# Kernel tuning notes

Measured on AMD Instinct MI355X. Metric: run time of the kernel, lower is better.

## Reference

```python
import jax, jax.numpy as jnp
import numpy as np

ALPHA = 3.0      # tanhalpha
K = 10           # subgraph_size (overridden to 10 in __init__)
PROP_ALPHA = 0.05
DEPTH = 2        # gcn_depth
NUM_FEAT = 2


def _build_graph(emb1, emb2, w1, b1, w2, b2):
    # MTGNN graph_constructor: directed adjacency + row-wise top-k sparsification
    n1 = jnp.tanh(ALPHA * (emb1 @ w1 + b1))
    n2 = jnp.tanh(ALPHA * (emb2 @ w2 + b2))
    a = n1 @ n2.T - n2 @ n1.T
    adj = jax.nn.relu(jnp.tanh(ALPHA * a))          # [N, N]
    _, idx = jax.lax.top_k(adj, K)                  # keep top-K per row
    N = adj.shape[0]
    mask = jnp.zeros_like(adj).at[jnp.arange(N)[:, None], idx].set(1.0)
    return adj * mask


def _norm_adj(adj):
    a = adj + jnp.eye(adj.shape[0], dtype=adj.dtype)
    return a / a.sum(axis=1, keepdims=True)


def _mixprop(x, a_norm, w, b):
    # x: [B, C, N, L]; multi-hop diffusion then 1x1 conv over stacked hops
    h = x
    outs = [x]
    for _ in range(DEPTH):
        h = PROP_ALPHA * x + (1.0 - PROP_ALPHA) * jnp.einsum('bcwl,vw->bcvl', h, a_norm)
        outs.append(h)
    ho = jnp.concatenate(outs, axis=1)              # [B, (D+1)C, N, L]
    return jnp.einsum('bcnl,oc->bonl', ho, w) + b[None, :, None, None]


def _conv1x1(x, w, b):
    # 1x1 Conv2d over channel dim of [B, C, N, L]
    return jnp.einsum('bcnl,oc->bonl', x, w) + b[None, :, None, None]


def _forward(history_data, node_emb_u, T_i_D_emb, D_i_W_emb,
             gc_emb1, gc_emb2, gc_w1, gc_b1, gc_w2, gc_b2,
             W_emb, b_emb, Wg1, bg1, Wg2, bg2, Wsc, bsc,
             mix1_w, mix1_b, mix2_w, mix2_b,
             Wtf1, btf1, Wtf2, btf2, Wec1, bec1, Wec2, bec2,
             Wfc1, bfc1, Wfc2, bfc2, Wec3, bec3):
    # --- prepare inputs ---
    tid_idx = (history_data[..., NUM_FEAT] * 288.0).astype(jnp.int32)   # [B,T,N]
    diw_idx = history_data[..., NUM_FEAT + 1].astype(jnp.int32)
    tid = T_i_D_emb[tid_idx]                                            # [B,T,N,TE]
    diw = D_i_W_emb[diw_idx]                                            # [B,T,N,TE]
    hd = history_data[..., :NUM_FEAT]                                   # [B,T,N,F]

    adj = _build_graph(gc_emb1, gc_emb2, gc_w1, gc_b1, gc_w2, gc_b2)    # [N,N]

    hd = hd @ W_emb + b_emb                                             # [B,T,N,H]
    B, T, N, H = hd.shape

    # --- decouple gate 1 ---
    nu = jnp.broadcast_to(node_emb_u[None, None], (B, T, N, node_emb_u.shape[-1]))
    g_in = jnp.concatenate([nu, tid, diw], axis=-1)                     # [B,T,N,64]
    gate = jax.nn.sigmoid(jax.nn.relu(g_in @ Wg1 + bg1) @ Wg2 + bg2)    # [B,T,N,H]
    x1 = gate * hd
    x2 = hd - x1
    gated = jnp.concatenate([x1, x2], axis=-1)                          # [B,T,N,2H]

    # start conv acts on the T(=12) dim as channels
    x1 = jax.nn.relu(jnp.einsum('btnh,ot->bonh', x1, Wsc) + bsc[None, :, None, None])
    x2 = jax.nn.relu(jnp.einsum('btnh,ot->bonh', x2, Wsc) + bsc[None, :, None, None])

    aN = _norm_adj(adj)
    aTN = _norm_adj(adj.T)
    outs = []
    for i in range(2):
        H1 = _mixprop(x1, aN, mix1_w[i], mix1_b[i]) + _mixprop(x1, aTN, mix2_w[i], mix2_b[i])
        H2 = _mixprop(x2, aN, mix1_w[i], mix1_b[i]) + _mixprop(x2, aTN, mix2_w[i], mix2_b[i])
        outs.append(H1)
        outs.append(H2)
    out = jnp.concatenate(outs, axis=-1)                                # [B,32,N,4H]

    # TFModule: 2-layer MLP on last dim (dropout = identity in eval)
    x = jax.nn.relu(out @ Wtf1 + btf1) @ Wtf2 + btf2                    # [B,32,N,4H]

    x = jax.nn.relu(_conv1x1(x, Wec1, bec1))                            # [B,128,N,4H]
    x = _conv1x1(x, Wec2, bec2)                                         # [B,12,N,4H]

    fh = jnp.concatenate([gated, x, tid, diw, hd], axis=-1)             # [B,12,N,472]
    f = jax.nn.relu(jax.nn.relu(fh) @ Wfc1 + bfc1) @ Wfc2 + bfc2        # [B,12,N,gap]
    f = _conv1x1(f, Wec3, bec3)                                         # [B,4,N,gap]
    f = jnp.transpose(f, (0, 2, 1, 3)).reshape(B, N, -1)                # [B,N,12]
    return f


def setup_inputs() -> dict:
    key = jax.random.key(0)
    ks = iter(jax.random.split(key, 48))
    def p(*shape, s=0.1):
        return (jax.random.normal(next(ks), shape, jnp.float32) * s)
    B, T, N, F_, H, ND, TE = 8, 12, 1024, 2, 64, 40, 12
    feat = jax.random.normal(next(ks), (B, T, N, F_), jnp.float32)
    tid = jax.random.uniform(next(ks), (B, T, N, 1), jnp.float32)
    diw = jax.random.randint(next(ks), (B, T, N, 1), 0, 7).astype(jnp.float32)
    history_data = jnp.concatenate([feat, tid, diw], axis=-1)
    return {
        'history_data': history_data,
        'node_emb_u': p(N, ND), 'T_i_D_emb': p(288, TE), 'D_i_W_emb': p(7, TE),
        'gc_emb1': p(N, ND), 'gc_emb2': p(N, ND),
        'gc_w1': p(ND, ND), 'gc_b1': jnp.zeros((ND,), jnp.float32),
        'gc_w2': p(ND, ND), 'gc_b2': jnp.zeros((ND,), jnp.float32),
        'W_emb': p(F_, H), 'b_emb': jnp.zeros((H,), jnp.float32),
        'Wg1': p(ND + 2 * TE, 64), 'bg1': jnp.zeros((64,), jnp.float32),
        'Wg2': p(64, H), 'bg2': jnp.zeros((H,), jnp.float32),
        'Wsc': p(32, T), 'bsc': jnp.zeros((32,), jnp.float32),
        'mix1_w': p(2, 32, 96), 'mix1_b': jnp.zeros((2, 32), jnp.float32),
        'mix2_w': p(2, 32, 96), 'mix2_b': jnp.zeros((2, 32), jnp.float32),
        'Wtf1': p(4 * H, 256, s=0.05), 'btf1': jnp.zeros((256,), jnp.float32),
        'Wtf2': p(256, 4 * H, s=0.05), 'btf2': jnp.zeros((4 * H,), jnp.float32),
        'Wec1': p(128, 32), 'bec1': jnp.zeros((128,), jnp.float32),
        'Wec2': p(12, 128), 'bec2': jnp.zeros((12,), jnp.float32),
        'Wfc1': p(472, 512, s=0.05), 'bfc1': jnp.zeros((512,), jnp.float32),
        'Wfc2': p(512, 3, s=0.05), 'bfc2': jnp.zeros((3,), jnp.float32),
        'Wec3': p(4, 12), 'bec3': jnp.zeros((4,), jnp.float32),
    }


def reference(history_data, node_emb_u, T_i_D_emb, D_i_W_emb,
              gc_emb1, gc_emb2, gc_w1, gc_b1, gc_w2, gc_b2,
              W_emb, b_emb, Wg1, bg1, Wg2, bg2, Wsc, bsc,
              mix1_w, mix1_b, mix2_w, mix2_b,
              Wtf1, btf1, Wtf2, btf2, Wec1, bec1, Wec2, bec2,
              Wfc1, bfc1, Wfc2, bfc2, Wec3, bec3):
    return _forward(history_data, node_emb_u, T_i_D_emb, D_i_W_emb,
                    gc_emb1, gc_emb2, gc_w1, gc_b1, gc_w2, gc_b2,
                    W_emb, b_emb, Wg1, bg1, Wg2, bg2, Wsc, bsc,
                    mix1_w, mix1_b, mix2_w, mix2_b,
                    Wtf1, btf1, Wtf2, btf2, Wec1, bec1, Wec2, bec2,
                    Wfc1, bfc1, Wfc2, bfc2, Wec3, bec3)
```

## Files before the change

kernel.cpp:

```cpp
#include <hip/hip_runtime.h>
#include <math.h>

constexpr int ROWS_PER_B = 12 * 1024;

constexpr size_t F_N1 = 0;
constexpr size_t F_N2 = 40960;
constexpr size_t F_ANVAL = 81920;
constexpr size_t F_ROWVAL = 93184;
constexpr size_t F_COLSUM = 103424;
constexpr size_t F_INVCS = 104448;
constexpr size_t F_ATVAL = 105472;
constexpr size_t I_ANIDX = 115712;
constexpr size_t I_ROWIDX = 126976;
constexpr size_t I_COLCNT = 137216;
constexpr size_t I_COLOFF = 138240;
constexpr size_t I_COLFILL = 139265;
constexpr size_t I_ATIDX = 140289;
constexpr size_t F_W1P = 151552;
constexpr size_t F_W2P = 184320;
constexpr size_t F_WFCP = 217088;
constexpr size_t F_WEC1P = 339968;
constexpr size_t F_WEC2P = 342016;
constexpr size_t F_WMWP = 343040;
constexpr size_t GRAPH_FLOATS = 524288;

constexpr size_t PB_GATED = (size_t)ROWS_PER_B * 128 / 2;
constexpr size_t PB_HD = (size_t)ROWS_PER_B * 64 / 2;
constexpr size_t PB_X = (size_t)32 * 1024 * 64 / 2;
constexpr size_t PB_MIX = (size_t)32 * 1024 * 256 / 2;
constexpr size_t PB_APK = (size_t)768 * 15 * 64 * 8 / 2;
constexpr size_t PB_TOTAL = PB_GATED + PB_HD + 5 * PB_X + PB_MIX + PB_APK;

typedef __attribute__((ext_vector_type(8))) short bf16x8;
typedef __attribute__((ext_vector_type(4))) float f32x4;

__device__ __forceinline__ unsigned short f2bf(float f) {
    unsigned u = __float_as_uint(f);
    unsigned r = (u + 0x7fffu + ((u >> 16) & 1u)) >> 16;
    return (unsigned short)r;
}
__device__ __forceinline__ float bf2f(unsigned short h) {
    return __uint_as_float((unsigned)h << 16);
}
__device__ __forceinline__ void unpack8(uint4 raw, float* f) {
    f[0] = bf2f((unsigned short)(raw.x & 0xffff)); f[1] = bf2f((unsigned short)(raw.x >> 16));
    f[2] = bf2f((unsigned short)(raw.y & 0xffff)); f[3] = bf2f((unsigned short)(raw.y >> 16));
    f[4] = bf2f((unsigned short)(raw.z & 0xffff)); f[5] = bf2f((unsigned short)(raw.z >> 16));
    f[6] = bf2f((unsigned short)(raw.w & 0xffff)); f[7] = bf2f((unsigned short)(raw.w >> 16));
}
__device__ __forceinline__ uint4 pack8(const float* f) {
    uint4 r;
    r.x = f2bf(f[0]) | ((unsigned)f2bf(f[1]) << 16);
    r.y = f2bf(f[2]) | ((unsigned)f2bf(f[3]) << 16);
    r.z = f2bf(f[4]) | ((unsigned)f2bf(f[5]) << 16);
    r.w = f2bf(f[6]) | ((unsigned)f2bf(f[7]) << 16);
    return r;
}
__device__ __forceinline__ bf16x8 relu8(bf16x8 v) {
#pragma unroll
    for (int j = 0; j < 8; j++) {
        unsigned short u = (unsigned short)v[j];
        v[j] = (short)((u >> 15) ? 0 : u);
    }
    return v;
}


__global__ void k_init(int* cnt, int* fill, float* csum) {
    int t = blockIdx.x * 256 + threadIdx.x;
    if (t < 1024) { cnt[t] = 0; fill[t] = 0; csum[t] = 0.f; }
}

__global__ void k_embed(const float* e1, const float* e2, const float* w1, const float* b1,
                        const float* w2, const float* b2, float* n1, float* n2) {
    int idx = blockIdx.x * 256 + threadIdx.x;
    if (idx >= 81920) return;
    int m = idx / 40960, rem = idx - m * 40960;
    int i = rem / 40, j = rem - i * 40;
    const float* e = m ? e2 : e1;
    const float* w = m ? w2 : w1;
    const float* bv = m ? b2 : b1;
    float a = bv[j];
    for (int k = 0; k < 40; k++) a += e[i * 40 + k] * w[k * 40 + j];
    (m ? n2 : n1)[i * 40 + j] = tanhf(3.0f * a);
}

__global__ __launch_bounds__(256) void k_adj(const float* n1, const float* n2,
        float* aN_val, int* aN_idx, float* row_val, int* row_idx,
        int* col_cnt, float* col_sum) {
    __shared__ float arow[1024];
    __shared__ float n1v[40], n2v[40];
    __shared__ float rv[256];
    __shared__ int ri[256];
    __shared__ float topv[10];
    __shared__ int topi[10];
    int v = blockIdx.x, t = threadIdx.x;
    if (t < 40) { n1v[t] = n1[v * 40 + t]; n2v[t] = n2[v * 40 + t]; }
    __syncthreads();
    for (int j = t; j < 1024; j += 256) {
        float d1 = 0.f, d2 = 0.f;
        for (int k = 0; k < 40; k++) {
            d1 += n1v[k] * n2[j * 40 + k];
            d2 += n2v[k] * n1[j * 40 + k];
        }
        float a = tanhf(3.0f * (d1 - d2));
        arow[j] = a > 0.f ? a : 0.f;
    }
    __syncthreads();
    for (int r = 0; r < 10; r++) {
        float bv = -1.f; int bi = 1 << 30;
        for (int j = t; j < 1024; j += 256) {
            float x = arow[j];
            if (x > bv || (x == bv && j < bi)) { bv = x; bi = j; }
        }
        rv[t] = bv; ri[t] = bi;
        __syncthreads();
        for (int s = 128; s > 0; s >>= 1) {
            if (t < s) {
                float ov = rv[t + s]; int oi = ri[t + s];
                if (ov > rv[t] || (ov == rv[t] && oi < ri[t])) { rv[t] = ov; ri[t] = oi; }
            }
            __syncthreads();
        }
        if (t == 0) { topv[r] = rv[0]; topi[r] = ri[0]; arow[ri[0]] = -1.f; }
        __syncthreads();
    }
    if (t == 0) {
        float s = 1.f;
        for (int r = 0; r < 10; r++) s += topv[r];
        float inv = 1.f / s;
        for (int r = 0; r < 10; r++) {
            aN_idx[v * 11 + r] = topi[r];
            aN_val[v * 11 + r] = topv[r] * inv;
            row_idx[v * 10 + r] = topi[r];
            row_val[v * 10 + r] = topv[r];
            atomicAdd(&col_cnt[topi[r]], 1);
            atomicAdd(&col_sum[topi[r]], topv[r]);
        }
        aN_idx[v * 11 + 10] = v;
        aN_val[v * 11 + 10] = inv;
    }
}

__global__ __launch_bounds__(1024) void k_scan(const int* cnt, int* off,
                                               const float* csum, float* inv) {
    __shared__ int tmp[1024];
    int t = threadIdx.x;
    tmp[t] = cnt[t];
    __syncthreads();
    for (int s = 1; s < 1024; s <<= 1) {
        int v = 0;
        if (t >= s) v = tmp[t - s];
        __syncthreads();
        tmp[t] += v;
        __syncthreads();
    }
    off[t + 1] = tmp[t];
    if (t == 0) off[0] = 0;
    inv[t] = 1.0f / (csum[t] + 1.0f);
}

__global__ void k_scatter(const int* row_idx, const float* row_val, const int* off,
                          int* fill, int* aT_idx, float* aT_val) {
    int e = blockIdx.x * 256 + threadIdx.x;
    if (e >= 10240) return;
    int v = e / 10;
    int j = row_idx[e];
    int pos = off[j] + atomicAdd(&fill[j], 1);
    aT_idx[pos] = v;
    aT_val[pos] = row_val[e];
}

__global__ void k_packw(const float* W, unsigned short* out) {
    int id = blockIdx.x * 256 + threadIdx.x;
    if (id >= 8192) return;
    int lane = id & 63, rest = id >> 6;
    int nb = rest & 15, kb = rest >> 4;
    int krow = kb * 32 + (lane >> 4) * 8;
    int col = nb * 16 + (lane & 15);
    unsigned short v[8];
#pragma unroll
    for (int j = 0; j < 8; j++) v[j] = f2bf(W[(size_t)(krow + j) * 256 + col]);
#pragma unroll
    for (int j = 0; j < 8; j++) out[(size_t)id * 8 + j] = v[j];
}

__global__ void k_packfc(const float* W, unsigned short* out) {
    int id = blockIdx.x * 256 + threadIdx.x;
    if (id >= 30720) return;
    int lane = id & 63, rest = id >> 6;
    int nb = rest & 31, kb = rest >> 5;
    int k0 = kb * 32 + (lane >> 4) * 8;
    int col = nb * 16 + (lane & 15);
    unsigned short v[8];
#pragma unroll
    for (int j = 0; j < 8; j++) {
        int k = k0 + j;
        v[j] = (k < 472) ? f2bf(W[(size_t)k * 512 + col]) : (unsigned short)0;
    }
#pragma unroll
    for (int j = 0; j < 8; j++) out[(size_t)id * 8 + j] = v[j];
}

__global__ void k_packec(const float* W1, const float* W2,
                         unsigned short* o1, unsigned short* o2) {
    int id = blockIdx.x * 256 + threadIdx.x;
    if (id < 512) {
        int mt = id >> 6, lane = id & 63;
        int o = mt * 16 + (lane & 15);
        int c0 = (lane >> 4) * 8;
#pragma unroll
        for (int j = 0; j < 8; j++)
            o1[(size_t)id * 8 + j] = f2bf(W1[o * 32 + c0 + j]);
    } else if (id < 768) {
        int id2 = id - 512;
        int kb = id2 >> 6, lane = id2 & 63;
        int p = lane & 15;
        int k0 = kb * 32 + (lane >> 4) * 8;
#pragma unroll
        for (int j = 0; j < 8; j++)
            o2[(size_t)id2 * 8 + j] = (p < 12) ? f2bf(W2[p * 128 + k0 + j])
                                               : (unsigned short)0;
    }
}

__global__ void k_packmw(const float* mw1, const float* mw2, unsigned short* out) {
    int id = blockIdx.x * 256 + threadIdx.x;
    if (id >= 1536) return;
    int f = id >> 6, lane = id & 63;
    int kb = f >> 2, rt = f & 3;
    int row = rt * 16 + (lane & 15);
    int ph = (kb >= 3) ? 1 : 0;
    int kloc = (kb - ph * 3) * 32 + (lane >> 4) * 8;
    const float* mw = ph ? mw2 : mw1;
#pragma unroll
    for (int j = 0; j < 8; j++)
        out[(size_t)id * 8 + j] = f2bf(mw[row * 96 + kloc + j]);
}


__global__ __launch_bounds__(256) void k_gate(const float* hist, const float* nodeu,
        const float* tide, const float* diwe,
        const float* Wg1, const float* bg1, const float* Wg2, const float* bg2,
        const float* Wemb, const float* bemb, unsigned short* gated, unsigned short* hd_emb) {
    __shared__ float w1[4096], w2[4096];
    __shared__ float gin[4][64], hid[4][64];
    __shared__ float sb1[64], sb2[64], we[128], be[64];
    int t = threadIdx.x;
    for (int i = t; i < 4096; i += 256) { w1[i] = Wg1[i]; w2[i] = Wg2[i]; }
    if (t < 64) { sb1[t] = bg1[t]; sb2[t] = bg2[t]; be[t] = bemb[t]; }
    if (t < 128) we[t] = Wemb[t];
    int r = t >> 6, lane = t & 63;
    int row = blockIdx.x * 4 + r;
    int n = row & 1023;
    const float* hrow = hist + (size_t)row * 4;
    float f0 = hrow[0], f1 = hrow[1];
    int tid_i = (int)(hrow[2] * 288.0f);
    int diw_i = (int)hrow[3];
    float g;
    if (lane < 40) g = nodeu[n * 40 + lane];
    else if (lane < 52) g = tide[tid_i * 12 + lane - 40];
    else g = diwe[diw_i * 12 + lane - 52];
    gin[r][lane] = g;
    __syncthreads();
    float acc = sb1[lane];
    for (int k = 0; k < 64; k++) acc += gin[r][k] * w1[k * 64 + lane];
    hid[r][lane] = acc > 0.f ? acc : 0.f;
    __syncthreads();
    acc = sb2[lane];
    for (int k = 0; k < 64; k++) acc += hid[r][k] * w2[k * 64 + lane];
    float gate = 1.f / (1.f + expf(-acc));
    float hd = f0 * we[lane] + f1 * we[64 + lane] + be[lane];
    float x1 = gate * hd;
    gated[(size_t)row * 128 + lane] = f2bf(x1);
    gated[(size_t)row * 128 + 64 + lane] = f2bf(hd - x1);
    hd_emb[(size_t)row * 64 + lane] = f2bf(hd);
}

__global__ __launch_bounds__(256) void k_wsc(const unsigned short* gated, const float* Wsc,
                                             const float* bsc, unsigned short* xs, int xoff) {
    __shared__ float w[384];
    __shared__ float sb[32];
    int t = threadIdx.x;
    if (t < 384) w[t] = Wsc[t];
    if (t < 32) sb[t] = bsc[t];
    __syncthreads();
    int idx = blockIdx.x * 256 + t;
    int h = idx & 63, n = (idx >> 6) & 1023, b = idx >> 16;
    float xv[12];
#pragma unroll
    for (int tt = 0; tt < 12; tt++)
        xv[tt] = bf2f(gated[(size_t)((b * 12 + tt) * 1024 + n) * 128 + xoff + h]);
#pragma unroll
    for (int o = 0; o < 32; o++) {
        float a = sb[o];
#pragma unroll
        for (int tt = 0; tt < 12; tt++) a += xv[tt] * w[o * 12 + tt];
        xs[(size_t)((b * 32 + o) * 1024 + n) * 64 + h] = f2bf(a > 0.f ? a : 0.f);
    }
}

__global__ __launch_bounds__(256) void k_spmm2(unsigned short* out1, unsigned short* out2,
        const unsigned short* x, const unsigned short* hin1, const unsigned short* hin2,
        const int* aN_idx, const float* aN_val,
        const int* aT_idx, const float* aT_val,
        const int* off, const float* inv_cs) {
    int nper = gridDim.x >> 3;
    int bid = (blockIdx.x & 7) * nper + (blockIdx.x >> 3);
    int t = threadIdx.x;
    int l8 = t & 7, r = t >> 3;
    int g = bid * 32 + r;
    int v = g & 1023, bc = g >> 10;
    size_t rowoff = (size_t)bc * 65536;
    float hv[8];
    const unsigned short* base1 = hin1 + rowoff;
    float s1[8];
#pragma unroll
    for (int j = 0; j < 8; j++) s1[j] = 0.f;
#pragma unroll
    for (int e = 0; e < 11; e++) {
        int w = aN_idx[v * 11 + e];
        float a = aN_val[v * 11 + e];
        uint4 raw = *(const uint4*)(base1 + (size_t)w * 64 + l8 * 8);
        unpack8(raw, hv);
#pragma unroll
        for (int j = 0; j < 8; j++) s1[j] += a * hv[j];
    }
    const unsigned short* base2 = hin2 + rowoff;
    float s2[8];
    {
        uint4 raw = *(const uint4*)(base2 + (size_t)v * 64 + l8 * 8);
        unpack8(raw, s2);
        int e0 = off[v], e1 = off[v + 1];
        for (int e = e0; e < e1; e++) {
            int w = aT_idx[e];
            float a = aT_val[e];
            uint4 rw = *(const uint4*)(base2 + (size_t)w * 64 + l8 * 8);
            unpack8(rw, hv);
#pragma unroll
            for (int j = 0; j < 8; j++) s2[j] += a * hv[j];
        }
        float ic = inv_cs[v];
#pragma unroll
        for (int j = 0; j < 8; j++) s2[j] *= ic;
    }
    uint4 xr = *(const uint4*)(x + (size_t)g * 64 + l8 * 8);
    float xv[8];
    unpack8(xr, xv);
    float o1[8], o2[8];
#pragma unroll
    for (int j = 0; j < 8; j++) {
        float xb = 0.05f * xv[j];
        o1[j] = xb + 0.95f * s1[j];
        o2[j] = xb + 0.95f * s2[j];
    }
    *(uint4*)(out1 + (size_t)g * 64 + l8 * 8) = pack8(o1);
    *(uint4*)(out2 + (size_t)g * 64 + l8 * 8) = pack8(o2);
}

__global__ __launch_bounds__(256) void k_proj(const unsigned short* xs,
        const unsigned short* h1, const unsigned short* h2,
        const unsigned short* h1b, const unsigned short* h2b,
        const unsigned short* mwp, const float* m1b, const float* m2b,
        unsigned short* mix, int xp) {
    __shared__ unsigned short Bf[24 * 64 * 8];
    int t = threadIdx.x;
    int wave = t >> 6, l = t & 63;
    int lr = l & 15, lg = l >> 4;
    int b = blockIdx.x >> 10, n = blockIdx.x & 1023;
#pragma unroll
    for (int i = 0; i < 6; i++) {
        int f = wave * 6 + i;
        int kb = f >> 2, nt = f & 3;
        int ph = (kb >= 3) ? 1 : 0;
        int q = kb - ph * 3;
        const unsigned short* Hq = (q == 0) ? xs : (q == 1 ? (ph ? h1b : h1)
                                                           : (ph ? h2b : h2));
        const unsigned short* src = Hq + ((size_t)(b * 32 + lg * 8) * 1024 + n) * 64
                                       + nt * 16 + lr;
        bf16x8 v;
#pragma unroll
        for (int j = 0; j < 8; j++)
            v[j] = (short)src[(size_t)j * 65536];
        *(bf16x8*)(Bf + ((size_t)f * 64 + l) * 8) = v;
    }
    __syncthreads();
    f32x4 acc[4];
#pragma unroll
    for (int nt = 0; nt < 4; nt++) {
        f32x4 c;
#pragma unroll
        for (int r = 0; r < 4; r++) {
            int row = wave * 16 + lg * 4 + r;
            c[r] = m1b[row] + m2b[row];
        }
        acc[nt] = c;
    }
#pragma unroll
    for (int kb = 0; kb < 6; kb++) {
        bf16x8 af = *(const bf16x8*)(mwp + (size_t)((kb * 4 + wave) * 64 + l) * 8);
#pragma unroll
        for (int nt = 0; nt < 4; nt++) {
            bf16x8 bfv = *(const bf16x8*)(Bf + ((size_t)(kb * 4 + nt) * 64 + l) * 8);
            acc[nt] = __builtin_amdgcn_mfma_f32_16x16x32_bf16(af, bfv, acc[nt], 0, 0, 0);
        }
    }
#pragma unroll
    for (int nt = 0; nt < 4; nt++)
#pragma unroll
        for (int r = 0; r < 4; r++) {
            int row = wave * 16 + lg * 4 + r;
            int i2 = row >> 5, o = row & 31;
            mix[(size_t)((b * 32 + o) * 1024 + n) * 256 + (i2 * 2 + xp) * 64 + nt * 16 + lr]
                = f2bf(acc[nt][r]);
        }
}

__global__ __launch_bounds__(256) void k_tf(unsigned short* mix, const unsigned short* W1p,
                                            const float* B1, const unsigned short* W2p,
                                            const float* B2) {
    __shared__ unsigned short Abuf[32 * 256];
    __shared__ unsigned short Hbuf[32 * 256];
    int t = threadIdx.x;
    int wave = t >> 6, l = t & 63;
    size_t row0 = (size_t)blockIdx.x * 32;
    const uint4* src = (const uint4*)(mix + row0 * 256);
#pragma unroll
    for (int it = 0; it < 4; it++) {
        int f = t + it * 256;
        uint4 raw = src[f];
        int e = f * 8, row = e >> 8, col = e & 255;
        int byte = (row * 512 + col * 2) ^ ((row & 7) << 4);
        *(uint4*)((char*)Abuf + byte) = raw;
    }
    __syncthreads();
    int colg0 = wave * 64;
    int lr = l & 15, lg = l >> 4;
    f32x4 acc[2][4];
#pragma unroll
    for (int nb = 0; nb < 4; nb++) {
        float bv = B1[colg0 + nb * 16 + lr];
        f32x4 c; c[0] = bv; c[1] = bv; c[2] = bv; c[3] = bv;
        acc[0][nb] = c; acc[1][nb] = c;
    }
#pragma unroll
    for (int kb = 0; kb < 8; kb++) {
        int k2 = (kb * 32 + lg * 8) * 2;
        int by0 = (lr * 512 + k2) ^ ((lr & 7) << 4);
        int by1 = ((16 + lr) * 512 + k2) ^ ((lr & 7) << 4);
        bf16x8 a0 = *(const bf16x8*)((char*)Abuf + by0);
        bf16x8 a1 = *(const bf16x8*)((char*)Abuf + by1);
#pragma unroll
        for (int nb = 0; nb < 4; nb++) {
            int nbg = wave * 4 + nb;
            bf16x8 bw = *(const bf16x8*)(W1p + (size_t)((kb * 16 + nbg) * 64 + l) * 8);
            acc[0][nb] = __builtin_amdgcn_mfma_f32_16x16x32_bf16(a0, bw, acc[0][nb], 0, 0, 0);
            acc[1][nb] = __builtin_amdgcn_mfma_f32_16x16x32_bf16(a1, bw, acc[1][nb], 0, 0, 0);
        }
    }
#pragma unroll
    for (int rb = 0; rb < 2; rb++)
#pragma unroll
        for (int nb = 0; nb < 4; nb++)
#pragma unroll
            for (int r = 0; r < 4; r++) {
                int row = rb * 16 + lg * 4 + r;
                int col = colg0 + nb * 16 + lr;
                unsigned short h = f2bf(fmaxf(acc[rb][nb][r], 0.f));
                int byte = (row * 512 + col * 2) ^ ((row & 7) << 4);
                *(unsigned short*)((char*)Hbuf + byte) = h;
            }
    __syncthreads();
#pragma unroll
    for (int nb = 0; nb < 4; nb++) {
        float bv = B2[colg0 + nb * 16 + lr];
        f32x4 c; c[0] = bv; c[1] = bv; c[2] = bv; c[3] = bv;
        acc[0][nb] = c; acc[1][nb] = c;
    }
#pragma unroll
    for (int kb = 0; kb < 8; kb++) {
        int k2 = (kb * 32 + lg * 8) * 2;
        int by0 = (lr * 512 + k2) ^ ((lr & 7) << 4);
        int by1 = ((16 + lr) * 512 + k2) ^ ((lr & 7) << 4);
        bf16x8 a0 = *(const bf16x8*)((char*)Hbuf + by0);
        bf16x8 a1 = *(const bf16x8*)((char*)Hbuf + by1);
#pragma unroll
        for (int nb = 0; nb < 4; nb++) {
            int nbg = wave * 4 + nb;
            bf16x8 bw = *(const bf16x8*)(W2p + (size_t)((kb * 16 + nbg) * 64 + l) * 8);
            acc[0][nb] = __builtin_amdgcn_mfma_f32_16x16x32_bf16(a0, bw, acc[0][nb], 0, 0, 0);
            acc[1][nb] = __builtin_amdgcn_mfma_f32_16x16x32_bf16(a1, bw, acc[1][nb], 0, 0, 0);
        }
    }
#pragma unroll
    for (int rb = 0; rb < 2; rb++)
#pragma unroll
        for (int nb = 0; nb < 4; nb++)
#pragma unroll
            for (int r = 0; r < 4; r++) {
                int row = rb * 16 + lg * 4 + r;
                int col = colg0 + nb * 16 + lr;
                mix[(row0 + row) * 256 + col] = f2bf(acc[rb][nb][r]);
            }
}

__global__ __launch_bounds__(256) void k_ec(const unsigned short* tfo,
        const unsigned short* W1p, const float* B1,
        const unsigned short* W2p, const float* B2, unsigned short* eco) {
    __shared__ unsigned short Hl[4 * 64 * 48];
    int t = threadIdx.x;
    int wave = t >> 6, l = t & 63;
    int lr = l & 15, lg = l >> 4;
    int b = blockIdx.x >> 10, n = blockIdx.x & 1023;
    int lbase = wave * 64;
    unsigned short* myH = Hl + wave * 3072;
    const unsigned short* xb = tfo + ((size_t)(b * 32) * 1024 + n) * 256;
    bf16x8 xf[4];
#pragma unroll
    for (int nt = 0; nt < 4; nt++) {
        int ll = lbase + nt * 16 + lr;
        bf16x8 v;
#pragma unroll
        for (int j = 0; j < 8; j++)
            v[j] = (short)xb[(size_t)(lg * 8 + j) * 262144 + ll];
        xf[nt] = v;
    }
    f32x4 d2[4];
    {
        f32x4 c;
#pragma unroll
        for (int r = 0; r < 4; r++) {
            int p = lg * 4 + r;
            c[r] = (p < 12) ? B2[p] : 0.f;
        }
#pragma unroll
        for (int nt = 0; nt < 4; nt++) d2[nt] = c;
    }
#pragma unroll
    for (int ch = 0; ch < 4; ch++) {
        f32x4 h[2][4];
#pragma unroll
        for (int mt = 0; mt < 2; mt++) {
            f32x4 c;
#pragma unroll
            for (int r = 0; r < 4; r++) c[r] = B1[ch * 32 + mt * 16 + lg * 4 + r];
#pragma unroll
            for (int nt = 0; nt < 4; nt++) h[mt][nt] = c;
        }
#pragma unroll
        for (int mt = 0; mt < 2; mt++) {
            bf16x8 aw = *(const bf16x8*)(W1p + (size_t)((ch * 2 + mt) * 64 + l) * 8);
#pragma unroll
            for (int nt = 0; nt < 4; nt++)
                h[mt][nt] = __builtin_amdgcn_mfma_f32_16x16x32_bf16(aw, xf[nt], h[mt][nt], 0, 0, 0);
        }
#pragma unroll
        for (int mt = 0; mt < 2; mt++)
#pragma unroll
            for (int nt = 0; nt < 4; nt++) {
                unsigned lo = f2bf(fmaxf(h[mt][nt][0], 0.f)) |
                              ((unsigned)f2bf(fmaxf(h[mt][nt][1], 0.f)) << 16);
                unsigned hi = f2bf(fmaxf(h[mt][nt][2], 0.f)) |
                              ((unsigned)f2bf(fmaxf(h[mt][nt][3], 0.f)) << 16);
                uint2 pk; pk.x = lo; pk.y = hi;
                *(uint2*)(myH + (nt * 16 + lr) * 48 + mt * 16 + lg * 4) = pk;
            }
        bf16x8 aw2 = *(const bf16x8*)(W2p + (size_t)(ch * 64 + l) * 8);
#pragma unroll
        for (int nt = 0; nt < 4; nt++) {
            bf16x8 hf = *(const bf16x8*)(myH + (nt * 16 + lr) * 48 + lg * 8);
            d2[nt] = __builtin_amdgcn_mfma_f32_16x16x32_bf16(aw2, hf, d2[nt], 0, 0, 0);
        }
    }
#pragma unroll
    for (int nt = 0; nt < 4; nt++)
#pragma unroll
        for (int r = 0; r < 4; r++) {
            int p = lg * 4 + r;
            if (p < 12) {
                int ll = lbase + nt * 16 + lr;
                eco[((size_t)(b * 12 + p) * 1024 + n) * 256 + ll] = f2bf(d2[nt][r]);
            }
        }
}

__global__ __launch_bounds__(256) void k_stage(const unsigned short* gated,
        const unsigned short* eco, const unsigned short* hd_emb,
        const float* hist, const float* tide, const float* diwe,
        unsigned short* apk) {
    int id = blockIdx.x * 256 + threadIdx.x;
    int lane = id & 63, rest = id >> 6;
    int rg = rest / 15, kb = rest - rg * 15;
    int lr = lane & 15, lg = lane >> 4;
    int grow = rg * 16 + lr;
    int n = grow & 1023, bt = grow >> 10;
    int b = bt / 12, tt = bt - b * 12;
    int off = kb * 32 + lg * 8;
    bf16x8 v;
    if (kb <= 3) {
        v = relu8(*(const bf16x8*)(gated + (size_t)grow * 128 + off));
    } else if (kb <= 11) {
        v = relu8(*(const bf16x8*)(eco + (size_t)((b * 12 + tt) * 1024 + n) * 256 + off - 128));
    } else if (kb == 12) {
        int tid_i = (int)(hist[(size_t)grow * 4 + 2] * 288.0f);
        int diw_i = (int)hist[(size_t)grow * 4 + 3];
        const unsigned short* hptr = hd_emb + (size_t)grow * 64;
#pragma unroll
        for (int j = 0; j < 8; j++) {
            int k = off + j;
            float x;
            if (k < 396) x = tide[tid_i * 12 + k - 384];
            else if (k < 408) x = diwe[diw_i * 12 + k - 396];
            else x = bf2f(hptr[k - 408]);
            v[j] = (short)f2bf(fmaxf(x, 0.f));
        }
    } else if (kb == 13) {
        v = relu8(*(const bf16x8*)(hd_emb + (size_t)grow * 64 + off - 408));
    } else {
        if (lg < 3) v = relu8(*(const bf16x8*)(hd_emb + (size_t)grow * 64 + off - 408));
        else {
#pragma unroll
            for (int j = 0; j < 8; j++) v[j] = 0;
        }
    }
    *(bf16x8*)(apk + (size_t)id * 8) = v;
}

__global__ __launch_bounds__(256) void k_fc(const unsigned short* apk,
        const unsigned short* W1p, const float* B1, const float* W2,
        float* pbuf) {
    int t = threadIdx.x;
    int wave = t >> 6, l = t & 63;
    int lr = l & 15, lg = l >> 4;
    int rg = blockIdx.x;
    int row0 = rg * 16;
    int colg0 = wave * 128;
    f32x4 acc[8];
#pragma unroll
    for (int nb = 0; nb < 8; nb++) {
        float bv = B1[colg0 + nb * 16 + lr];
        f32x4 c; c[0] = bv; c[1] = bv; c[2] = bv; c[3] = bv;
        acc[nb] = c;
    }
#pragma unroll
    for (int kb = 0; kb < 15; kb++) {
        bf16x8 af = *(const bf16x8*)(apk + (size_t)((rg * 15 + kb) * 64 + l) * 8);
#pragma unroll
        for (int nb = 0; nb < 8; nb++) {
            bf16x8 bw = *(const bf16x8*)(W1p + (size_t)((kb * 32 + wave * 8 + nb) * 64 + l) * 8);
            acc[nb] = __builtin_amdgcn_mfma_f32_16x16x32_bf16(af, bw, acc[nb], 0, 0, 0);
        }
    }
    float p[4][3];
#pragma unroll
    for (int r = 0; r < 4; r++) { p[r][0] = 0.f; p[r][1] = 0.f; p[r][2] = 0.f; }
#pragma unroll
    for (int nb = 0; nb < 8; nb++) {
        int col = colg0 + nb * 16 + lr;
        float w0 = W2[col * 3], w1 = W2[col * 3 + 1], w2 = W2[col * 3 + 2];
#pragma unroll
        for (int r = 0; r < 4; r++) {
            float h = fmaxf(acc[nb][r], 0.f);
            p[r][0] += h * w0; p[r][1] += h * w1; p[r][2] += h * w2;
        }
    }
#pragma unroll
    for (int off = 8; off >= 1; off >>= 1)
#pragma unroll
        for (int r = 0; r < 4; r++) {
            p[r][0] += __shfl_xor(p[r][0], off);
            p[r][1] += __shfl_xor(p[r][1], off);
            p[r][2] += __shfl_xor(p[r][2], off);
        }
    if (lr == 0) {
#pragma unroll
        for (int r = 0; r < 4; r++) {
            size_t gr = (size_t)(row0 + lg * 4 + r);
#pragma unroll
            for (int pp = 0; pp < 3; pp++)
                pbuf[gr * 12 + wave * 3 + pp] = p[r][pp];
        }
    }
}

__global__ void k_ec3(const float* pbuf, const float* B2, const float* W, const float* bv,
                      float* out) {
    int idx = blockIdx.x * 256 + threadIdx.x;
    int l = idx % 3;
    int rest = idx / 3;
    int o = rest & 3;
    int n = (rest >> 2) & 1023;
    int b = rest >> 12;
    float s = bv[o];
#pragma unroll
    for (int c = 0; c < 12; c++) {
        const float* pb = pbuf + ((size_t)(b * 12 + c) * 1024 + n) * 12;
        float fv = B2[l] + pb[l] + pb[3 + l] + pb[6 + l] + pb[9 + l];
        s += fv * W[o * 12 + c];
    }
    out[idx] = s;
}

extern "C" void kernel_launch(void* const* d_in, const int* in_sizes, int n_in,
                              void* d_out, int out_size, void* d_ws, size_t ws_size,
                              hipStream_t stream) {
    const float* hist = (const float*)d_in[0];
    const float* node_emb_u = (const float*)d_in[1];
    const float* T_i_D_emb = (const float*)d_in[2];
    const float* D_i_W_emb = (const float*)d_in[3];
    const float* gc_emb1 = (const float*)d_in[4];
    const float* gc_emb2 = (const float*)d_in[5];
    const float* gc_w1 = (const float*)d_in[6];
    const float* gc_b1 = (const float*)d_in[7];
    const float* gc_w2 = (const float*)d_in[8];
    const float* gc_b2 = (const float*)d_in[9];
    const float* W_emb = (const float*)d_in[10];
    const float* b_emb = (const float*)d_in[11];
    const float* Wg1 = (const float*)d_in[12];
    const float* bg1 = (const float*)d_in[13];
    const float* Wg2 = (const float*)d_in[14];
    const float* bg2 = (const float*)d_in[15];
    const float* Wsc = (const float*)d_in[16];
    const float* bsc = (const float*)d_in[17];
    const float* mix1_w = (const float*)d_in[18];
    const float* mix1_b = (const float*)d_in[19];
    const float* mix2_w = (const float*)d_in[20];
    const float* mix2_b = (const float*)d_in[21];
    const float* Wtf1 = (const float*)d_in[22];
    const float* btf1 = (const float*)d_in[23];
    const float* Wtf2 = (const float*)d_in[24];
    const float* btf2 = (const float*)d_in[25];
    const float* Wec1 = (const float*)d_in[26];
    const float* bec1 = (const float*)d_in[27];
    const float* Wec2 = (const float*)d_in[28];
    const float* bec2 = (const float*)d_in[29];
    const float* Wfc1 = (const float*)d_in[30];
    const float* bfc1 = (const float*)d_in[31];
    const float* Wfc2 = (const float*)d_in[32];
    const float* bfc2 = (const float*)d_in[33];
    const float* Wec3 = (const float*)d_in[34];
    const float* bec3 = (const float*)d_in[35];

    float* ws = (float*)d_ws;
    float* n1 = ws + F_N1;
    float* n2 = ws + F_N2;
    float* aN_val = ws + F_ANVAL;
    float* row_val = ws + F_ROWVAL;
    float* col_sum = ws + F_COLSUM;
    float* inv_cs = ws + F_INVCS;
    float* aT_val = ws + F_ATVAL;
    int* aN_idx = (int*)(ws + I_ANIDX);
    int* row_idx = (int*)(ws + I_ROWIDX);
    int* col_cnt = (int*)(ws + I_COLCNT);
    int* col_off = (int*)(ws + I_COLOFF);
    int* col_fill = (int*)(ws + I_COLFILL);
    int* aT_idx = (int*)(ws + I_ATIDX);
    unsigned short* w1p = (unsigned short*)(ws + F_W1P);
    unsigned short* w2p = (unsigned short*)(ws + F_W2P);
    unsigned short* wfcp = (unsigned short*)(ws + F_WFCP);
    unsigned short* wec1p = (unsigned short*)(ws + F_WEC1P);
    unsigned short* wec2p = (unsigned short*)(ws + F_WEC2P);
    unsigned short* wmwp = (unsigned short*)(ws + F_WMWP);

    size_t avail = ws_size / 4;
    int CB = 8;
    while (CB > 1 && GRAPH_FLOATS + (size_t)CB * PB_TOTAL > avail) CB >>= 1;
    int nchunk = 8 / CB;

    unsigned short* gated = (unsigned short*)(ws + GRAPH_FLOATS);
    unsigned short* hd_emb = (unsigned short*)(ws + GRAPH_FLOATS + (size_t)CB * PB_GATED);
    unsigned short* xs = (unsigned short*)(ws + GRAPH_FLOATS + (size_t)CB * (PB_GATED + PB_HD));
    unsigned short* h1 = xs + (size_t)CB * PB_X * 2;
    unsigned short* h2 = h1 + (size_t)CB * PB_X * 2;
    unsigned short* h1b = h2 + (size_t)CB * PB_X * 2;
    unsigned short* h2b = h1b + (size_t)CB * PB_X * 2;
    unsigned short* mix = h2b + (size_t)CB * PB_X * 2;
    unsigned short* apk = mix + (size_t)CB * PB_MIX * 2;
    unsigned short* eco = xs;
    float* fbuf = (float*)h2b;

    k_init<<<4, 256, 0, stream>>>(col_cnt, col_fill, col_sum);
    k_embed<<<320, 256, 0, stream>>>(gc_emb1, gc_emb2, gc_w1, gc_b1, gc_w2, gc_b2, n1, n2);
    k_adj<<<1024, 256, 0, stream>>>(n1, n2, aN_val, aN_idx, row_val, row_idx, col_cnt, col_sum);
    k_scan<<<1, 1024, 0, stream>>>(col_cnt, col_off, col_sum, inv_cs);
    k_scatter<<<40, 256, 0, stream>>>(row_idx, row_val, col_off, col_fill, aT_idx, aT_val);
    k_packw<<<32, 256, 0, stream>>>(Wtf1, w1p);
    k_packw<<<32, 256, 0, stream>>>(Wtf2, w2p);
    k_packfc<<<120, 256, 0, stream>>>(Wfc1, wfcp);
    k_packec<<<3, 256, 0, stream>>>(Wec1, Wec2, wec1p, wec2p);
    k_packmw<<<6, 256, 0, stream>>>(mix1_w, mix2_w, wmwp);

    for (int ch = 0; ch < nchunk; ch++) {
        const float* hist_c = hist + (size_t)ch * CB * ROWS_PER_B * 4;
        float* out_c = (float*)d_out + (size_t)ch * CB * ROWS_PER_B;

        k_gate<<<CB * 3072, 256, 0, stream>>>(hist_c, node_emb_u, T_i_D_emb, D_i_W_emb,
                                              Wg1, bg1, Wg2, bg2, W_emb, b_emb, gated, hd_emb);
        for (int xp = 0; xp < 2; xp++) {
            k_wsc<<<CB * 256, 256, 0, stream>>>(gated, Wsc, bsc, xs, xp * 64);
            k_spmm2<<<CB * 1024, 256, 0, stream>>>(h1, h1b, xs, xs, xs,
                                                   aN_idx, aN_val, aT_idx, aT_val,
                                                   col_off, inv_cs);
            k_spmm2<<<CB * 1024, 256, 0, stream>>>(h2, h2b, xs, h1, h1b,
                                                   aN_idx, aN_val, aT_idx, aT_val,
                                                   col_off, inv_cs);
            k_proj<<<CB * 1024, 256, 0, stream>>>(xs, h1, h2, h1b, h2b,
                                                  wmwp, mix1_b, mix2_b, mix, xp);
        }
        k_tf<<<CB * 1024, 256, 0, stream>>>(mix, w1p, btf1, w2p, btf2);
        k_ec<<<CB * 1024, 256, 0, stream>>>(mix, wec1p, bec1, wec2p, bec2, eco);
        k_stage<<<CB * 2880, 256, 0, stream>>>(gated, eco, hd_emb, hist_c,
                                               T_i_D_emb, D_i_W_emb, apk);
        k_fc<<<CB * 768, 256, 0, stream>>>(apk, wfcp, bfc1, Wfc2, fbuf);
        k_ec3<<<CB * 48, 256, 0, stream>>>(fbuf, bfc2, Wec3, bec3, out_c);
    }
}
```

Measured before the change: 1.185 ms.

## Fuse both mixprop diffusion hops into one LDS-resident kernel per channel slice

```diff
diff --git a/kernel.cpp b/kernel.cpp
--- a/kernel.cpp
+++ b/kernel.cpp
@@ -300,62 +300,109 @@
     }
 }
 
-__global__ __launch_bounds__(256) void k_spmm2(unsigned short* out1, unsigned short* out2,
-        const unsigned short* x, const unsigned short* hin1, const unsigned short* hin2,
+__global__ __launch_bounds__(1024) void k_mixprop(const unsigned short* xs,
+        unsigned short* h1, unsigned short* h2,
+        unsigned short* h1b, unsigned short* h2b,
         const int* aN_idx, const float* aN_val,
         const int* aT_idx, const float* aT_val,
         const int* off, const float* inv_cs) {
+    extern __shared__ char smem[];
+    unsigned short* S0 = (unsigned short*)smem;
+    unsigned short* S1 = S0 + 1024 * 24;
     int nper = gridDim.x >> 3;
     int bid = (blockIdx.x & 7) * nper + (blockIdx.x >> 3);
-    int t = threadIdx.x;
-    int l8 = t & 7, r = t >> 3;
-    int g = bid * 32 + r;
-    int v = g & 1023, bc = g >> 10;
-    size_t rowoff = (size_t)bc * 65536;
-    float hv[8];
-    const unsigned short* base1 = hin1 + rowoff;
-    float s1[8];
-#pragma unroll
-    for (int j = 0; j < 8; j++) s1[j] = 0.f;
+    int bc = bid >> 2, q = bid & 3;
+    int c0 = q * 16;
+    int v = threadIdx.x;
+    size_t rowbase = ((size_t)bc * 1024 + v) * 64 + c0;
+    uint4 r0 = *(const uint4*)(xs + rowbase);
+    uint4 r1 = *(const uint4*)(xs + rowbase + 8);
+    float xv[16];
+    unpack8(r0, xv);
+    unpack8(r1, xv + 8);
+    *(uint4*)(S0 + v * 24) = r0;
+    *(uint4*)(S0 + v * 24 + 8) = r1;
+    int ei[11]; float ev[11];
+#pragma unroll
+    for (int e = 0; e < 11; e++) { ei[e] = aN_idx[v * 11 + e]; ev[e] = aN_val[v * 11 + e]; }
+    int e0 = off[v], e1 = off[v + 1];
+    float ic = inv_cs[v];
+    __syncthreads();
+    float o1[16], o1b[16], hvv[16];
+#pragma unroll
+    for (int j = 0; j < 16; j++) o1[j] = 0.f;
 #pragma unroll
     for (int e = 0; e < 11; e++) {
-        int w = aN_idx[v * 11 + e];
-        float a = aN_val[v * 11 + e];
-        uint4 raw = *(const uint4*)(base1 + (size_t)w * 64 + l8 * 8);
-        unpack8(raw, hv);
-#pragma unroll
-        for (int j = 0; j < 8; j++) s1[j] += a * hv[j];
-    }
-    const unsigned short* base2 = hin2 + rowoff;
-    float s2[8];
+        const unsigned short* sp = S0 + ei[e] * 24;
+        uint4 g0 = *(const uint4*)sp;
+        uint4 g1 = *(const uint4*)(sp + 8);
+        unpack8(g0, hvv); unpack8(g1, hvv + 8);
+        float a = ev[e];
+#pragma unroll
+        for (int j = 0; j < 16; j++) o1[j] += a * hvv[j];
+    }
+#pragma unroll
+    for (int j = 0; j < 16; j++) o1[j] = 0.05f * xv[j] + 0.95f * o1[j];
+#pragma unroll
+    for (int j = 0; j < 16; j++) o1b[j] = xv[j];
+    for (int e = e0; e < e1; e++) {
+        const unsigned short* sp = S0 + aT_idx[e] * 24;
+        float a = aT_val[e];
+        uint4 g0 = *(const uint4*)sp;
+        uint4 g1 = *(const uint4*)(sp + 8);
+        unpack8(g0, hvv); unpack8(g1, hvv + 8);
+#pragma unroll
+        for (int j = 0; j < 16; j++) o1b[j] += a * hvv[j];
+    }
+#pragma unroll
+    for (int j = 0; j < 16; j++) o1b[j] = 0.05f * xv[j] + 0.95f * ic * o1b[j];
+    uint4 p10 = pack8(o1), p11 = pack8(o1 + 8);
+    uint4 pb0 = pack8(o1b), pb1 = pack8(o1b + 8);
+    *(uint4*)(h1 + rowbase) = p10;
+    *(uint4*)(h1 + rowbase + 8) = p11;
+    *(uint4*)(h1b + rowbase) = pb0;
+    *(uint4*)(h1b + rowbase + 8) = pb1;
+    __syncthreads();
+    *(uint4*)(S1 + v * 24) = p10;
+    *(uint4*)(S1 + v * 24 + 8) = p11;
+    *(uint4*)(S0 + v * 24) = pb0;
+    *(uint4*)(S0 + v * 24 + 8) = pb1;
+    __syncthreads();
+#pragma unroll
+    for (int j = 0; j < 16; j++) o1[j] = 0.f;
+#pragma unroll
+    for (int e = 0; e < 11; e++) {
+        const unsigned short* sp = S1 + ei[e] * 24;
+        uint4 g0 = *(const uint4*)sp;
+        uint4 g1 = *(const uint4*)(sp + 8);
+        unpack8(g0, hvv); unpack8(g1, hvv + 8);
+        float a = ev[e];
+#pragma unroll
+        for (int j = 0; j < 16; j++) o1[j] += a * hvv[j];
+    }
+#pragma unroll
+    for (int j = 0; j < 16; j++) o1[j] = 0.05f * xv[j] + 0.95f * o1[j];
     {
-        uint4 raw = *(const uint4*)(base2 + (size_t)v * 64 + l8 * 8);
-        unpack8(raw, s2);
-        int e0 = off[v], e1 = off[v + 1];
-        for (int e = e0; e < e1; e++) {
-            int w = aT_idx[e];
-            float a = aT_val[e];
-            uint4 rw = *(const uint4*)(base2 + (size_t)w * 64 + l8 * 8);
-            unpack8(rw, hv);
-#pragma unroll
-            for (int j = 0; j < 8; j++) s2[j] += a * hv[j];
-        }
-        float ic = inv_cs[v];
-#pragma unroll
-        for (int j = 0; j < 8; j++) s2[j] *= ic;
-    }
-    uint4 xr = *(const uint4*)(x + (size_t)g * 64 + l8 * 8);
-    float xv[8];
-    unpack8(xr, xv);
-    float o1[8], o2[8];
-#pragma unroll
-    for (int j = 0; j < 8; j++) {
-        float xb = 0.05f * xv[j];
-        o1[j] = xb + 0.95f * s1[j];
-        o2[j] = xb + 0.95f * s2[j];
-    }
-    *(uint4*)(out1 + (size_t)g * 64 + l8 * 8) = pack8(o1);
-    *(uint4*)(out2 + (size_t)g * 64 + l8 * 8) = pack8(o2);
+        const unsigned short* sp = S0 + v * 24;
+        uint4 g0 = *(const uint4*)sp;
+        uint4 g1 = *(const uint4*)(sp + 8);
+        unpack8(g0, o1b); unpack8(g1, o1b + 8);
+    }
+    for (int e = e0; e < e1; e++) {
+        const unsigned short* sp = S0 + aT_idx[e] * 24;
+        float a = aT_val[e];
+        uint4 g0 = *(const uint4*)sp;
+        uint4 g1 = *(const uint4*)(sp + 8);
+        unpack8(g0, hvv); unpack8(g1, hvv + 8);
+#pragma unroll
+        for (int j = 0; j < 16; j++) o1b[j] += a * hvv[j];
+    }
+#pragma unroll
+    for (int j = 0; j < 16; j++) o1b[j] = 0.05f * xv[j] + 0.95f * ic * o1b[j];
+    *(uint4*)(h2 + rowbase) = pack8(o1);
+    *(uint4*)(h2 + rowbase + 8) = pack8(o1 + 8);
+    *(uint4*)(h2b + rowbase) = pack8(o1b);
+    *(uint4*)(h2b + rowbase + 8) = pack8(o1b + 8);
 }
 
 __global__ __launch_bounds__(256) void k_proj(const unsigned short* xs,
@@ -798,12 +845,9 @@
                                               Wg1, bg1, Wg2, bg2, W_emb, b_emb, gated, hd_emb);
         for (int xp = 0; xp < 2; xp++) {
             k_wsc<<<CB * 256, 256, 0, stream>>>(gated, Wsc, bsc, xs, xp * 64);
-            k_spmm2<<<CB * 1024, 256, 0, stream>>>(h1, h1b, xs, xs, xs,
-                                                   aN_idx, aN_val, aT_idx, aT_val,
-                                                   col_off, inv_cs);
-            k_spmm2<<<CB * 1024, 256, 0, stream>>>(h2, h2b, xs, h1, h1b,
-                                                   aN_idx, aN_val, aT_idx, aT_val,
-                                                   col_off, inv_cs);
+            k_mixprop<<<CB * 128, 1024, 98304, stream>>>(xs, h1, h2, h1b, h2b,
+                                                         aN_idx, aN_val, aT_idx, aT_val,
+                                                         col_off, inv_cs);
             k_proj<<<CB * 1024, 256, 0, stream>>>(xs, h1, h2, h1b, h2b,
                                                   wmwp, mix1_b, mix2_b, mix, xp);
         }
```

After: 1.431 ms. 20.8% more time.
